# Kernel tuning notes

Measured on AMD Instinct MI355X. Metric: run time of the kernel, lower is better.

The kernel has to match this reference:

```python
import jax, jax.numpy as jnp
import numpy as np

N_NODES = 50000
N_EDGES = 600000
DIM = 128
BN_EPS = 1e-5


def _gine_conv(x, src, dst, edge_attr, W, b):
    # message: relu(x_j + e_ij), gathered from source nodes
    m = jax.nn.relu(x[src] + edge_attr)              # [E, D]
    aggr = jax.ops.segment_sum(m, dst, num_segments=x.shape[0])  # [N, D]
    # eps = 0 (PyG default, train_eps=False): (1+eps)*x + aggr
    return (x + aggr) @ W.T + b


def _batchnorm(x, gamma, beta):
    mean = jnp.mean(x, axis=0)
    var = jnp.var(x, axis=0)
    return (x - mean) * jax.lax.rsqrt(var + BN_EPS) * gamma + beta


def setup_inputs() -> dict:
    key = jax.random.key(0)
    ks = jax.random.split(key, 16)
    scale = 1.0 / np.sqrt(DIM)
    inp = {
        "edge_index": jax.random.randint(ks[0], (2, N_EDGES), 0, N_NODES, dtype=jnp.int64 if jax.config.jax_enable_x64 else jnp.int32),
        "node_attr": jax.random.normal(ks[1], (N_NODES, DIM), dtype=jnp.float32),
        "edge_attr": jax.random.normal(ks[2], (N_EDGES, DIM), dtype=jnp.float32),
    }
    for i in range(3):
        inp[f"W{i+1}"] = jax.random.uniform(ks[3 + i], (DIM, DIM), jnp.float32, -scale, scale)
        inp[f"b{i+1}"] = jax.random.uniform(ks[6 + i], (DIM,), jnp.float32, -scale, scale)
        inp[f"gamma{i+1}"] = jnp.ones((DIM,), jnp.float32)
        inp[f"beta{i+1}"] = jnp.zeros((DIM,), jnp.float32)
    return inp


def reference(edge_index, node_attr, edge_attr,
              W1, b1, gamma1, beta1,
              W2, b2, gamma2, beta2,
              W3, b3, gamma3, beta3):
    src, dst = edge_index[0], edge_index[1]
    x = jax.nn.relu(_gine_conv(node_attr, src, dst, edge_attr, W1, b1))
    x = _batchnorm(x, gamma1, beta1)
    x = jax.nn.relu(_gine_conv(x, src, dst, edge_attr, W2, b2))
    x = _batchnorm(x, gamma2, beta2)
    x = jax.nn.relu(_gine_conv(x, src, dst, edge_attr, W3, b3))
    x = _batchnorm(x, gamma3, beta3)
    return x
```

## Files before the change

### kernel.cpp

```cpp
#include <hip/hip_runtime.h>
#include <stdint.h>

#define NN 50000
#define NE 600000
#define DIM 128
#define BN_EPS 1e-5f
#define NCHUNK ((NN + 255) / 256)

typedef __attribute__((ext_vector_type(8))) short bf16x8;
typedef __attribute__((ext_vector_type(4))) float f32x4;

__device__ __forceinline__ unsigned short f2b(float f) {
    unsigned u = __float_as_uint(f);
    u += 0x7FFF + ((u >> 16) & 1);
    return (unsigned short)(u >> 16);
}
__device__ __forceinline__ float b2f(unsigned short h) {
    return __uint_as_float((unsigned)h << 16);
}


__global__ void count_k(const int* __restrict__ dst, int* __restrict__ counts, int E) {
    int i = blockIdx.x * 256 + threadIdx.x;
    if (i < E) atomicAdd(&counts[dst[i]], 1);
}

__global__ __launch_bounds__(256) void chunksum_k(const int* __restrict__ counts,
                                                  int* __restrict__ bsum) {
    __shared__ int lds[256];
    int i = blockIdx.x * 256 + threadIdx.x;
    lds[threadIdx.x] = (i < NN) ? counts[i] : 0;
    __syncthreads();
    for (int off = 128; off > 0; off >>= 1) {
        if (threadIdx.x < (unsigned)off) lds[threadIdx.x] += lds[threadIdx.x + off];
        __syncthreads();
    }
    if (threadIdx.x == 0) bsum[blockIdx.x] = lds[0];
}

__global__ __launch_bounds__(256) void chunkscan_k(const int* __restrict__ bsum,
                                                   int* __restrict__ bbase,
                                                   int* __restrict__ offsets) {
    __shared__ int lds[256];
    int t = threadIdx.x;
    int v = (t < NCHUNK) ? bsum[t] : 0;
    lds[t] = v;
    __syncthreads();
    for (int off = 1; off < 256; off <<= 1) {
        int a = (t >= (unsigned)off) ? lds[t - off] : 0;
        __syncthreads();
        lds[t] += a;
        __syncthreads();
    }
    if (t < NCHUNK) bbase[t] = lds[t] - v;
    if (t == 0) offsets[NN] = NE;
}

__global__ __launch_bounds__(256) void scatteroff_k(const int* __restrict__ counts,
                                                    const int* __restrict__ bbase,
                                                    int* __restrict__ offsets,
                                                    int* __restrict__ cursor) {
    __shared__ int lds[256];
    int t = threadIdx.x;
    int i = blockIdx.x * 256 + t;
    int v = (i < NN) ? counts[i] : 0;
    lds[t] = v;
    __syncthreads();
    for (int off = 1; off < 256; off <<= 1) {
        int a = (t >= (unsigned)off) ? lds[t - off] : 0;
        __syncthreads();
        lds[t] += a;
        __syncthreads();
    }
    if (i < NN) {
        int excl = bbase[blockIdx.x] + lds[t] - v;
        offsets[i] = excl;
        cursor[i] = excl;
    }
}

template <bool WEBF>
__global__ __launch_bounds__(256) void fillcvt_k(
        const int* __restrict__ dst, const int* __restrict__ src,
        const float* __restrict__ eattr, int* __restrict__ cursor,
        int* __restrict__ csrc, int* __restrict__ eidx,
        unsigned short* __restrict__ ebf) {
    int lane = threadIdx.x & 31;
    int g = blockIdx.x * 8 + (threadIdx.x >> 5);
    int base = g * 32;
    if (base >= NE) return;
    int i = base + lane;
    int d = dst[i];
    int p = atomicAdd(&cursor[d], 1);
    csrc[p] = src[i];
    eidx[p] = i;
    if (!WEBF) return;
    int f = lane * 4;
    for (int t = 0; t < 32; ++t) {
        int pt = __shfl(p, t, 32);
        float4 v = *(const float4*)(eattr + (size_t)(base + t) * DIM + f);
        ushort4 o = {f2b(v.x), f2b(v.y), f2b(v.z), f2b(v.w)};
        *(ushort4*)(ebf + (size_t)pt * DIM + f) = o;
    }
}

__global__ __launch_bounds__(256) void wcvt_k(const float* __restrict__ w0,
                                              const float* __restrict__ w1,
                                              const float* __restrict__ w2,
                                              unsigned short* __restrict__ whi,
                                              unsigned short* __restrict__ wlo) {
    int i = blockIdx.x * 256 + threadIdx.x;
    int which = i >> 12;
    int off = (i & 4095) * 4;
    const float* w = (which == 0) ? w0 : ((which == 1) ? w1 : w2);
    float4 v = *(const float4*)(w + off);
    ushort4 h = {f2b(v.x), f2b(v.y), f2b(v.z), f2b(v.w)};
    ushort4 l = {f2b(v.x - b2f(h.x)), f2b(v.y - b2f(h.y)),
                 f2b(v.z - b2f(h.z)), f2b(v.w - b2f(h.w))};
    *(ushort4*)(whi + (size_t)which * 16384 + off) = h;
    *(ushort4*)(wlo + (size_t)which * 16384 + off) = l;
}

template <int XMODE, int EMODE>
__global__ __launch_bounds__(256) void layer_k(
        const float* __restrict__ xf, const unsigned short* __restrict__ xb,
        const float* __restrict__ scale, const float* __restrict__ shift,
        const unsigned short* __restrict__ ebf, const float* __restrict__ eattr,
        const int* __restrict__ eidx, const int* __restrict__ offsets,
        const int* __restrict__ csrc,
        const unsigned short* __restrict__ whi, const unsigned short* __restrict__ wlo,
        const float* __restrict__ bias, unsigned short* __restrict__ yb,
        double* __restrict__ gsum, double* __restrict__ gsumsq) {
    __shared__ float sS[16][DIM + 4];
    __shared__ unsigned short ylds[16][136];

    int tid = threadIdx.x;
    int lane31 = tid & 31;
    int grp = tid >> 5;
    int n0 = blockIdx.x * 16;
    int f = lane31 * 4;

    float4 sc, sh;
    if (XMODE) {
        sc = *(const float4*)(scale + f);
        sh = *(const float4*)(shift + f);
    }

#pragma unroll
    for (int sub = 0; sub < 2; ++sub) {
        int n = n0 + grp * 2 + sub;
        float4 acc = make_float4(0.f, 0.f, 0.f, 0.f);
        int beg = offsets[n], end = offsets[n + 1];
        for (int b = beg; b < end; b += 32) {
            int kk = b + lane31;
            int s_l = (kk < end) ? csrc[kk] : 0;
            int e_l = 0;
            if (EMODE == 1) e_l = (kk < end) ? eidx[kk] : 0;
            int cnt = end - b;
            if (cnt > 32) cnt = 32;
#pragma unroll 4
            for (int t = 0; t < cnt; ++t) {
                int s = __shfl(s_l, t, 32);
                float4 ev;
                if (EMODE == 0) {
                    ushort4 eb = *(const ushort4*)(ebf + (size_t)(b + t) * DIM + f);
                    ev = make_float4(b2f(eb.x), b2f(eb.y), b2f(eb.z), b2f(eb.w));
                } else {
                    int e = __shfl(e_l, t, 32);
                    ev = *(const float4*)(eattr + (size_t)e * DIM + f);
                }
                float4 xv;
                if (XMODE == 0) {
                    xv = *(const float4*)(xf + (size_t)s * DIM + f);
                } else {
                    ushort4 u = *(const ushort4*)(xb + (size_t)s * DIM + f);
                    xv = make_float4(fmaf(b2f(u.x), sc.x, sh.x),
                                     fmaf(b2f(u.y), sc.y, sh.y),
                                     fmaf(b2f(u.z), sc.z, sh.z),
                                     fmaf(b2f(u.w), sc.w, sh.w));
                }
                acc.x += fmaxf(xv.x + ev.x, 0.f);
                acc.y += fmaxf(xv.y + ev.y, 0.f);
                acc.z += fmaxf(xv.z + ev.z, 0.f);
                acc.w += fmaxf(xv.w + ev.w, 0.f);
            }
        }
        float4 xn;
        if (XMODE == 0) {
            xn = *(const float4*)(xf + (size_t)n * DIM + f);
        } else {
            ushort4 u = *(const ushort4*)(xb + (size_t)n * DIM + f);
            xn = make_float4(fmaf(b2f(u.x), sc.x, sh.x), fmaf(b2f(u.y), sc.y, sh.y),
                             fmaf(b2f(u.z), sc.z, sh.z), fmaf(b2f(u.w), sc.w, sh.w));
        }
        float4 o = make_float4(xn.x + acc.x, xn.y + acc.y, xn.z + acc.z, xn.w + acc.w);
        *(float4*)(&sS[grp * 2 + sub][f]) = o;
    }
    __syncthreads();

    int wv = tid >> 6;
    int lane = tid & 63;
    int row = lane & 15;
    int kg = lane >> 4;
    int d0 = wv * 32;
    const unsigned short* bh = whi + (size_t)(d0 + row) * DIM + kg * 8;
    const unsigned short* bl = wlo + (size_t)(d0 + row) * DIM + kg * 8;

    f32x4 acc0 = {0.f, 0.f, 0.f, 0.f};
    f32x4 acc1 = {0.f, 0.f, 0.f, 0.f};
#pragma unroll
    for (int ks = 0; ks < 4; ++ks) {
        const float* ap = &sS[row][kg * 8 + ks * 32];
        bf16x8 ahi, alo;
#pragma unroll
        for (int j = 0; j < 8; ++j) {
            float av = ap[j];
            unsigned short h = f2b(av);
            ahi[j] = (short)h;
            alo[j] = (short)f2b(av - b2f(h));
        }
        bf16x8 b0h = *(const bf16x8*)(bh + ks * 32);
        bf16x8 b0l = *(const bf16x8*)(bl + ks * 32);
        bf16x8 b1h = *(const bf16x8*)(bh + 16 * DIM + ks * 32);
        bf16x8 b1l = *(const bf16x8*)(bl + 16 * DIM + ks * 32);
        acc0 = __builtin_amdgcn_mfma_f32_16x16x32_bf16(ahi, b0h, acc0, 0, 0, 0);
        acc0 = __builtin_amdgcn_mfma_f32_16x16x32_bf16(ahi, b0l, acc0, 0, 0, 0);
        acc0 = __builtin_amdgcn_mfma_f32_16x16x32_bf16(alo, b0h, acc0, 0, 0, 0);
        acc1 = __builtin_amdgcn_mfma_f32_16x16x32_bf16(ahi, b1h, acc1, 0, 0, 0);
        acc1 = __builtin_amdgcn_mfma_f32_16x16x32_bf16(ahi, b1l, acc1, 0, 0, 0);
        acc1 = __builtin_amdgcn_mfma_f32_16x16x32_bf16(alo, b1h, acc1, 0, 0, 0);
    }

    float bias0 = bias[d0 + row];
    float bias1 = bias[d0 + 16 + row];
    float s0 = 0.f, q0 = 0.f, s1 = 0.f, q1 = 0.f;
#pragma unroll
    for (int r = 0; r < 4; ++r) {
        int m = kg * 4 + r;
        float y0 = fmaxf(acc0[r] + bias0, 0.f);
        float y1 = fmaxf(acc1[r] + bias1, 0.f);
        ylds[m][d0 + row] = f2b(y0);
        ylds[m][d0 + 16 + row] = f2b(y1);
        s0 += y0; q0 += y0 * y0;
        s1 += y1; q1 += y1 * y1;
    }
    s0 += __shfl_xor(s0, 16); s0 += __shfl_xor(s0, 32);
    q0 += __shfl_xor(q0, 16); q0 += __shfl_xor(q0, 32);
    s1 += __shfl_xor(s1, 16); s1 += __shfl_xor(s1, 32);
    q1 += __shfl_xor(q1, 16); q1 += __shfl_xor(q1, 32);
    if (kg == 0) {
        atomicAdd(&gsum[d0 + row], (double)s0);
        atomicAdd(&gsumsq[d0 + row], (double)q0);
        atomicAdd(&gsum[d0 + 16 + row], (double)s1);
        atomicAdd(&gsumsq[d0 + 16 + row], (double)q1);
    }
    __syncthreads();
    int nrow = tid >> 4, seg = tid & 15;
    *(float4*)(yb + (size_t)(n0 + nrow) * DIM + seg * 8) =
        *(const float4*)(&ylds[nrow][seg * 8]);
}

__global__ void finalize_k(double* __restrict__ gsum, double* __restrict__ gsumsq,
                           const float* __restrict__ gamma, const float* __restrict__ beta,
                           float* __restrict__ scale, float* __restrict__ shift) {
    int d = threadIdx.x;
    if (d < DIM) {
        double mean = gsum[d] * (1.0 / NN);
        double var = gsumsq[d] * (1.0 / NN) - mean * mean;
        float sc = gamma[d] * rsqrtf((float)var + BN_EPS);
        scale[d] = sc;
        shift[d] = beta[d] - (float)mean * sc;
        gsum[d] = 0.0;
        gsumsq[d] = 0.0;
    }
}

__global__ __launch_bounds__(256) void norm_out_k(
        const unsigned short* __restrict__ yb, const float* __restrict__ scale,
        const float* __restrict__ shift, float* __restrict__ out) {
    int i = blockIdx.x * 256 + threadIdx.x;
    int f = (i & 31) * 4;
    ushort4 y = *(const ushort4*)(yb + (size_t)i * 4);
    float4 sc = *(const float4*)(scale + f);
    float4 sh = *(const float4*)(shift + f);
    float4 o;
    o.x = fmaf(b2f(y.x), sc.x, sh.x);
    o.y = fmaf(b2f(y.y), sc.y, sh.y);
    o.z = fmaf(b2f(y.z), sc.z, sh.z);
    o.w = fmaf(b2f(y.w), sc.w, sh.w);
    ((float4*)out)[i] = o;
}


extern "C" void kernel_launch(void* const* d_in, const int* in_sizes, int n_in,
                              void* d_out, int out_size, void* d_ws, size_t ws_size,
                              hipStream_t stream) {
    const int* edge_index = (const int*)d_in[0];
    const int* srcs = edge_index;
    const int* dsts = edge_index + NE;
    const float* node_attr = (const float*)d_in[1];
    const float* eattr = (const float*)d_in[2];
    const float* Wp[3]    = {(const float*)d_in[3],  (const float*)d_in[7],  (const float*)d_in[11]};
    const float* bp[3]    = {(const float*)d_in[4],  (const float*)d_in[8],  (const float*)d_in[12]};
    const float* gammap[3]= {(const float*)d_in[5],  (const float*)d_in[9],  (const float*)d_in[13]};
    const float* betap[3] = {(const float*)d_in[6],  (const float*)d_in[10], (const float*)d_in[14]};

    size_t off = 0;
    char* base = (char*)d_ws;
    auto carve = [&](size_t bytes) -> void* {
        void* p = base + off;
        off += (bytes + 255) & ~(size_t)255;
        return p;
    };
    unsigned short* ybufA = (unsigned short*)carve((size_t)NN * DIM * 2);
    unsigned short* ybufB = (unsigned short*)carve((size_t)NN * DIM * 2);
    int* csrc    = (int*)carve((size_t)NE * 4);
    int* eidx    = (int*)carve((size_t)NE * 4);
    int* offsets = (int*)carve((size_t)(NN + 1) * 4);
    int* cursor  = (int*)carve((size_t)NN * 4);
    int* bsum    = (int*)carve((size_t)NCHUNK * 4);
    int* bbase   = (int*)carve((size_t)NCHUNK * 4);
    int* counts  = (int*)carve((size_t)NN * 4);
    double* gsum = (double*)carve(DIM * 8);
    double* gsumsq = (double*)carve(DIM * 8);
    size_t zero_bytes = (size_t)((char*)gsumsq - (char*)counts) + DIM * 8;
    float* scb   = (float*)carve(3 * DIM * 4);
    float* shb   = (float*)carve(3 * DIM * 4);
    unsigned short* whi = (unsigned short*)carve(3 * DIM * DIM * 2);
    unsigned short* wlo = (unsigned short*)carve(3 * DIM * DIM * 2);
    int use_ebf = (off + (size_t)NE * DIM * 2 <= ws_size);
    unsigned short* ebf = use_ebf ? (unsigned short*)carve((size_t)NE * DIM * 2) : nullptr;

    hipMemsetAsync(counts, 0, zero_bytes, stream);
    count_k<<<(NE + 255) / 256, 256, 0, stream>>>(dsts, counts, NE);
    chunksum_k<<<NCHUNK, 256, 0, stream>>>(counts, bsum);
    chunkscan_k<<<1, 256, 0, stream>>>(bsum, bbase, offsets);
    scatteroff_k<<<NCHUNK, 256, 0, stream>>>(counts, bbase, offsets, cursor);
    if (use_ebf)
        fillcvt_k<true><<<(NE / 32 + 7) / 8, 256, 0, stream>>>(dsts, srcs, eattr, cursor,
                                                               csrc, eidx, ebf);
    else
        fillcvt_k<false><<<(NE / 32 + 7) / 8, 256, 0, stream>>>(dsts, srcs, eattr, cursor,
                                                                csrc, eidx, nullptr);
    wcvt_k<<<48, 256, 0, stream>>>(Wp[0], Wp[1], Wp[2], whi, wlo);

    if (use_ebf)
        layer_k<0, 0><<<NN / 16, 256, 0, stream>>>(node_attr, nullptr, nullptr, nullptr,
                                                   ebf, eattr, eidx, offsets, csrc,
                                                   whi, wlo, bp[0], ybufA, gsum, gsumsq);
    else
        layer_k<0, 1><<<NN / 16, 256, 0, stream>>>(node_attr, nullptr, nullptr, nullptr,
                                                   nullptr, eattr, eidx, offsets, csrc,
                                                   whi, wlo, bp[0], ybufA, gsum, gsumsq);
    finalize_k<<<1, DIM, 0, stream>>>(gsum, gsumsq, gammap[0], betap[0], scb, shb);

    unsigned short* xin = ybufA;
    unsigned short* yout = ybufB;
    for (int l = 1; l < 3; ++l) {
        const float* sc = scb + (l - 1) * DIM;
        const float* sh = shb + (l - 1) * DIM;
        if (use_ebf)
            layer_k<1, 0><<<NN / 16, 256, 0, stream>>>(nullptr, xin, sc, sh,
                                                       ebf, eattr, eidx, offsets, csrc,
                                                       whi + l * DIM * DIM, wlo + l * DIM * DIM,
                                                       bp[l], yout, gsum, gsumsq);
        else
            layer_k<1, 1><<<NN / 16, 256, 0, stream>>>(nullptr, xin, sc, sh,
                                                       nullptr, eattr, eidx, offsets, csrc,
                                                       whi + l * DIM * DIM, wlo + l * DIM * DIM,
                                                       bp[l], yout, gsum, gsumsq);
        finalize_k<<<1, DIM, 0, stream>>>(gsum, gsumsq, gammap[l], betap[l],
                                          scb + l * DIM, shb + l * DIM);
        unsigned short* t = xin; xin = yout; yout = t;
    }
    norm_out_k<<<NN * DIM / 4 / 256, 256, 0, stream>>>(xin, scb + 2 * DIM, shb + 2 * DIM,
                                                       (float*)d_out);
}
```

Before: 498.0 us.

## Drop activation low-part MFMA, skip eidx write, replace memset with zero kernel

The node-update GEMM no longer splits activations into hi/lo bf16 parts, which cuts the MFMA count from six to four per k-step and removes the residual conversion work, at some cost in accuracy. The fill kernel writes the edge index permutation only when the bf16 edge buffer is absent, saving a scattered store per edge. The host memset is replaced by a small zeroing kernel to avoid memset launch overhead.

```diff
diff --git a/kernel.cpp b/kernel.cpp
--- a/kernel.cpp
+++ b/kernel.cpp
@@ -19,6 +19,14 @@
     return __uint_as_float((unsigned)h << 16);
 }
 
+
+__global__ __launch_bounds__(256) void zero_k(int* __restrict__ counts,
+                                              double* __restrict__ gsum,
+                                              double* __restrict__ gsumsq) {
+    int i = blockIdx.x * 256 + threadIdx.x;
+    if (i < NN) counts[i] = 0;
+    if (i < DIM) { gsum[i] = 0.0; gsumsq[i] = 0.0; }
+}
 
 __global__ void count_k(const int* __restrict__ dst, int* __restrict__ counts, int E) {
     int i = blockIdx.x * 256 + threadIdx.x;
@@ -93,8 +101,7 @@
     int d = dst[i];
     int p = atomicAdd(&cursor[d], 1);
     csrc[p] = src[i];
-    eidx[p] = i;
-    if (!WEBF) return;
+    if (!WEBF) { eidx[p] = i; return; }
     int f = lane * 4;
     for (int t = 0; t < 32; ++t) {
         int pt = __shfl(p, t, 32);
@@ -211,24 +218,17 @@
 #pragma unroll
     for (int ks = 0; ks < 4; ++ks) {
         const float* ap = &sS[row][kg * 8 + ks * 32];
-        bf16x8 ahi, alo;
+        bf16x8 a;
 #pragma unroll
-        for (int j = 0; j < 8; ++j) {
-            float av = ap[j];
-            unsigned short h = f2b(av);
-            ahi[j] = (short)h;
-            alo[j] = (short)f2b(av - b2f(h));
-        }
+        for (int j = 0; j < 8; ++j) a[j] = (short)f2b(ap[j]);
         bf16x8 b0h = *(const bf16x8*)(bh + ks * 32);
         bf16x8 b0l = *(const bf16x8*)(bl + ks * 32);
         bf16x8 b1h = *(const bf16x8*)(bh + 16 * DIM + ks * 32);
         bf16x8 b1l = *(const bf16x8*)(bl + 16 * DIM + ks * 32);
-        acc0 = __builtin_amdgcn_mfma_f32_16x16x32_bf16(ahi, b0h, acc0, 0, 0, 0);
-        acc0 = __builtin_amdgcn_mfma_f32_16x16x32_bf16(ahi, b0l, acc0, 0, 0, 0);
-        acc0 = __builtin_amdgcn_mfma_f32_16x16x32_bf16(alo, b0h, acc0, 0, 0, 0);
-        acc1 = __builtin_amdgcn_mfma_f32_16x16x32_bf16(ahi, b1h, acc1, 0, 0, 0);
-        acc1 = __builtin_amdgcn_mfma_f32_16x16x32_bf16(ahi, b1l, acc1, 0, 0, 0);
-        acc1 = __builtin_amdgcn_mfma_f32_16x16x32_bf16(alo, b1h, acc1, 0, 0, 0);
+        acc0 = __builtin_amdgcn_mfma_f32_16x16x32_bf16(a, b0h, acc0, 0, 0, 0);
+        acc0 = __builtin_amdgcn_mfma_f32_16x16x32_bf16(a, b0l, acc0, 0, 0, 0);
+        acc1 = __builtin_amdgcn_mfma_f32_16x16x32_bf16(a, b1h, acc1, 0, 0, 0);
+        acc1 = __builtin_amdgcn_mfma_f32_16x16x32_bf16(a, b1l, acc1, 0, 0, 0);
     }
 
     float bias0 = bias[d0 + row];
@@ -323,7 +323,6 @@
     int* counts  = (int*)carve((size_t)NN * 4);
     double* gsum = (double*)carve(DIM * 8);
     double* gsumsq = (double*)carve(DIM * 8);
-    size_t zero_bytes = (size_t)((char*)gsumsq - (char*)counts) + DIM * 8;
     float* scb   = (float*)carve(3 * DIM * 4);
     float* shb   = (float*)carve(3 * DIM * 4);
     unsigned short* whi = (unsigned short*)carve(3 * DIM * DIM * 2);
@@ -331,7 +330,7 @@
     int use_ebf = (off + (size_t)NE * DIM * 2 <= ws_size);
     unsigned short* ebf = use_ebf ? (unsigned short*)carve((size_t)NE * DIM * 2) : nullptr;
 
-    hipMemsetAsync(counts, 0, zero_bytes, stream);
+    zero_k<<<NCHUNK, 256, 0, stream>>>(counts, gsum, gsumsq);
     count_k<<<(NE + 255) / 256, 256, 0, stream>>>(dsts, counts, NE);
     chunksum_k<<<NCHUNK, 256, 0, stream>>>(counts, bsum);
     chunkscan_k<<<1, 256, 0, stream>>>(bsum, bbase, offsets);
```

New measurement: 491.8 us. No clear change (-1.2%).
